# Performance work log

Hardware: AMD Instinct MI355X
Metric: run time of the kernel (lower is better)

The kernel has to match this reference:

```python
import jax, jax.numpy as jnp
import numpy as np

B, S, D = 2, 2048, 2048
H, HKV, HD = 32, 8, 64
G = H // HKV  # num_key_value_groups


def setup_inputs() -> dict:
    key = jax.random.key(0)
    ks = jax.random.split(key, 9)
    sc = 0.02
    return {
        "x": jax.random.normal(ks[0], (B, S, D), jnp.float32),
        "wq": jax.random.normal(ks[1], (H * HD, D), jnp.float32) * sc,
        "bq": jax.random.normal(ks[2], (H * HD,), jnp.float32) * sc,
        "wk": jax.random.normal(ks[3], (HKV * HD, D), jnp.float32) * sc,
        "bk": jax.random.normal(ks[4], (HKV * HD,), jnp.float32) * sc,
        "wv": jax.random.normal(ks[5], (HKV * HD, D), jnp.float32) * sc,
        "bv": jax.random.normal(ks[6], (HKV * HD,), jnp.float32) * sc,
        "wo": jax.random.normal(ks[7], (D, H * HD), jnp.float32) * sc,
        "bo": jax.random.normal(ks[8], (D,), jnp.float32) * sc,
    }


def reference(x, wq, bq, wk, bk, wv, bv, wo, bo):
    b, s, _ = x.shape
    # fused-QKV-style projections (nn.Linear: x @ W.T + b)
    q = (jnp.einsum("bsd,ed->bse", x, wq) + bq).reshape(b, s, H, HD)
    k = (jnp.einsum("bsd,ed->bse", x, wk) + bk).reshape(b, s, HKV, HD)
    v = (jnp.einsum("bsd,ed->bse", x, wv) + bv).reshape(b, s, HKV, HD)
    # (B, Hkv, G, S, hd): grouped query heads share a KV head — same math as
    # repeat_kv (expand+flatten) without materializing the expanded KV tensor
    q = q.transpose(0, 2, 1, 3).reshape(b, HKV, G, s, HD)
    k = k.transpose(0, 2, 1, 3)  # (B, Hkv, S, hd)
    v = v.transpose(0, 2, 1, 3)
    scale = 1.0 / jnp.sqrt(jnp.asarray(HD, x.dtype))
    scores = jnp.einsum("bkgqd,bktd->bkgqt", q, k) * scale  # (B,Hkv,G,S,S)
    causal = jnp.tril(jnp.ones((s, s), bool))
    scores = jnp.where(causal, scores, jnp.asarray(-jnp.inf, scores.dtype))
    probs = jax.nn.softmax(scores, axis=-1)
    o = jnp.einsum("bkgqt,bktd->bkgqd", probs, v)  # (B,Hkv,G,S,hd)
    o = o.reshape(b, H, s, HD).transpose(0, 2, 1, 3).reshape(b, s, H * HD)
    return jnp.einsum("bse,de->bsd", o, wo) + bo
```

## Files before the change

kernel.cpp:

```cpp
#include <hip/hip_runtime.h>
#include <hip/hip_bf16.h>
#include <cmath>

#define B_   2
#define S_   2048
#define D_   2048
#define H_   32
#define HKV_ 8
#define HD_  64

using bf16 = __hip_bfloat16;
typedef __bf16    bf16x8 __attribute__((ext_vector_type(8)));
typedef float     floatx4 __attribute__((ext_vector_type(4)));
typedef _Float16  half4 __attribute__((ext_vector_type(4)));
typedef _Float16  half8 __attribute__((ext_vector_type(8)));
typedef _Float16  half2v __attribute__((ext_vector_type(2)));

#if __has_builtin(__builtin_amdgcn_exp2f)
#define EXP2(x) __builtin_amdgcn_exp2f(x)
#else
#define EXP2(x) exp2f(x)
#endif

#define QSCALE 0.18033688011112042f

__device__ inline void async16(const void* g, void* l) {
  __builtin_amdgcn_global_load_lds(
      (const __attribute__((address_space(1))) void*)g,
      (__attribute__((address_space(3))) void*)l, 16, 0, 0);
}

__device__ inline half2v pkrtz(float a, float b) {
  return __builtin_bit_cast(half2v, __builtin_amdgcn_cvt_pkrtz(a, b));
}

#define MFMA32B(a, b, c) __builtin_amdgcn_mfma_f32_16x16x32_bf16((a), (b), (c), 0, 0, 0)
#define MFMA16H(a, b, c) __builtin_amdgcn_mfma_f32_16x16x16f16((a), (b), (c), 0, 0, 0)

#define BARX() { asm volatile("" ::: "memory"); __builtin_amdgcn_s_barrier(); \
                 asm volatile("" ::: "memory"); }
#define LGKM0() asm volatile("s_waitcnt lgkmcnt(0)" ::: "memory")

__global__ void f2b_all(const float* __restrict__ x,  const float* __restrict__ wq,
                        const float* __restrict__ wk, const float* __restrict__ wv,
                        const float* __restrict__ wo,
                        bf16* __restrict__ xb,  bf16* __restrict__ wqb,
                        bf16* __restrict__ wkb, bf16* __restrict__ wvb,
                        bf16* __restrict__ wob) {
  const int i = blockIdx.x * blockDim.x + threadIdx.x;
  const float* src; bf16* dst; int off; float scale = 1.0f;
  if (i < 1048576)      { src = x;  dst = xb;  off = 0; }
  else if (i < 1572864) { src = wq; dst = wqb; off = 1048576; scale = QSCALE; }
  else if (i < 1703936) { src = wk; dst = wkb; off = 1572864; }
  else if (i < 1835008) { src = wv; dst = wvb; off = 1703936; }
  else                  { src = wo; dst = wob; off = 1835008; }
  const int j = i - off;
  float4 a  = ((const float4*)src)[2 * j];
  float4 b2 = ((const float4*)src)[2 * j + 1];
  alignas(16) bf16 t[8];
  t[0] = __float2bfloat16(a.x * scale);  t[1] = __float2bfloat16(a.y * scale);
  t[2] = __float2bfloat16(a.z * scale);  t[3] = __float2bfloat16(a.w * scale);
  t[4] = __float2bfloat16(b2.x * scale); t[5] = __float2bfloat16(b2.y * scale);
  t[6] = __float2bfloat16(b2.z * scale); t[7] = __float2bfloat16(b2.w * scale);
  ((uint4*)dst)[j] = *(const uint4*)t;
}

__global__ __launch_bounds__(256, 2)
void gemm_qkv8(const bf16* __restrict__ xb, const bf16* __restrict__ Wcat,
               const float* __restrict__ bq, const float* __restrict__ bk,
               const float* __restrict__ bv,
               bf16* __restrict__ Qo, bf16* __restrict__ Ko,
               _Float16* __restrict__ VG) {
  constexpr int NT = D_ / 64;
  constexpr int BUFE = 20480;
  __shared__ bf16 L[2 * BUFE];

  const int id  = blockIdx.x;
  const int swz = (id & 7) * 64 + (id >> 3);
  const int bn  = swz >> 5;
  const int bm  = swz & 31;

  const int tid = threadIdx.x;
  const int wid = tid >> 6, lane = tid & 63;
  const int lm = lane & 15, quad = lane >> 4;
  const int wm = wid >> 1, wn = wid & 1;

  const int cOff = (quad * 8) ^ (((lm >> 3) & 1) << 4);
  const bf16* LA0 = L + (wm * 64 + lm) * 32 + cOff;
  const bf16* LB0 = L + 8192 + (wn * 96 + lm) * 32 + cOff;

  const int r0 = tid >> 2;
  const int csrc = ((tid & 3) * 8) ^ (((tid >> 5) & 1) << 4);
  const bf16* Asrc = xb   + (size_t)(bm * 128 + r0) * D_ + csrc;
  const bf16* Bsrc = Wcat + (size_t)(bn * 192 + r0) * D_ + csrc;
  bf16* Ld = L + tid * 8;

  floatx4 acc[4][6] = {};

#define STG_A(tt, hh, DB) { \
    async16(Asrc + (tt) * 64 + (hh) * 32,                  (DB) + (hh) * 4096); \
    async16(Asrc + (size_t)64 * D_ + (tt) * 64 + (hh) * 32, (DB) + (hh) * 4096 + 2048); }
#define STG_B(tt, hh, DB) { \
    async16(Bsrc + (tt) * 64 + (hh) * 32,                    (DB) + 8192 + (hh) * 6144); \
    async16(Bsrc + (size_t)64 * D_ + (tt) * 64 + (hh) * 32,  (DB) + 8192 + (hh) * 6144 + 2048); \
    async16(Bsrc + (size_t)128 * D_ + (tt) * 64 + (hh) * 32, (DB) + 8192 + (hh) * 6144 + 4096); }

  STG_A(0, 0, Ld); STG_B(0, 0, Ld);
  STG_A(0, 1, Ld); STG_B(0, 1, Ld);
  STG_A(1, 0, Ld + BUFE); STG_B(1, 0, Ld + BUFE);
  asm volatile("s_waitcnt vmcnt(10)" ::: "memory");
  BARX();

  auto tile = [&](int t, const int BUF) __attribute__((always_inline)) {
    const bf16* LA = LA0 + BUF;
    const bf16* LB = LB0 + BUF;
    bf16* SD  = Ld + BUF;
    bf16* SDo = Ld + (BUF ^ BUFE);
    const bool s1 = (t + 1) < NT, s2 = (t + 2) < NT;
    bf16x8 aF[4], bF[6];

#pragma unroll
    for (int i = 0; i < 4; ++i) aF[i] = *(const bf16x8*)(LA + i * 512);
#pragma unroll
    for (int i = 0; i < 6; ++i) bF[i] = *(const bf16x8*)(LB + i * 512);
    if (s1) { STG_A(t + 1, 1, SDo); STG_B(t + 1, 1, SDo); }
    BARX(); LGKM0();
    __builtin_amdgcn_s_setprio(1);
#pragma unroll
    for (int mi = 0; mi < 4; ++mi)
#pragma unroll
      for (int ni = 0; ni < 6; ++ni)
        acc[mi][ni] = MFMA32B(bF[ni], aF[mi], acc[mi][ni]);
    __builtin_amdgcn_s_setprio(0);
    if (s1) { asm volatile("s_waitcnt vmcnt(10)" ::: "memory"); }
    else    { asm volatile("s_waitcnt vmcnt(0)" ::: "memory"); }
    BARX();

#pragma unroll
    for (int i = 0; i < 4; ++i) aF[i] = *(const bf16x8*)(LA + 4096 + i * 512);
#pragma unroll
    for (int i = 0; i < 6; ++i) bF[i] = *(const bf16x8*)(LB + 6144 + i * 512);
    if (s2) { STG_A(t + 2, 0, SD); STG_B(t + 2, 0, SD); }
    BARX(); LGKM0();
    __builtin_amdgcn_s_setprio(1);
#pragma unroll
    for (int mi = 0; mi < 4; ++mi)
#pragma unroll
      for (int ni = 0; ni < 6; ++ni)
        acc[mi][ni] = MFMA32B(bF[ni], aF[mi], acc[mi][ni]);
    __builtin_amdgcn_s_setprio(0);
    if (s2)      { asm volatile("s_waitcnt vmcnt(10)" ::: "memory"); }
    else if (s1) { asm volatile("s_waitcnt vmcnt(5)" ::: "memory"); }
    else         { asm volatile("s_waitcnt vmcnt(0)" ::: "memory"); }
    BARX();
  };

  for (int t = 0; t < NT; t += 2) { tile(t, 0); tile(t + 1, BUFE); }

#undef STG_A
#undef STG_B

#pragma unroll
  for (int mi = 0; mi < 4; ++mi) {
    const int row = bm * 128 + wm * 64 + mi * 16 + lm;
#pragma unroll
    for (int ni = 0; ni < 6; ++ni) {
      const int colf = bn * 192 + wn * 96 + ni * 16;
      const int col0 = colf + quad * 4;
      if (colf < 2048) {
        float4 bv4 = *(const float4*)&bq[col0];
        alignas(8) bf16 t4[4];
#pragma unroll
        for (int r = 0; r < 4; ++r)
          t4[r] = __float2bfloat16(acc[mi][ni][r] + ((const float*)&bv4)[r] * QSCALE);
        *(uint2*)&Qo[(size_t)row * (H_ * HD_) + col0] = *(const uint2*)t4;
      } else if (colf < 2560) {
        const int ck = col0 - 2048;
        float4 bv4 = *(const float4*)&bk[ck];
        alignas(8) bf16 t4[4];
#pragma unroll
        for (int r = 0; r < 4; ++r)
          t4[r] = __float2bfloat16(acc[mi][ni][r] + ((const float*)&bv4)[r]);
        *(uint2*)&Ko[(size_t)row * (HKV_ * HD_) + ck] = *(const uint2*)t4;
      } else {
        const int cv = col0 - 2560;
        const int kvh = cv >> 6, hd = cv & 63;
        const int nh = hd >> 4;
        const int bb = row >> 11, s2 = row & 2047;
        const int tl = s2 >> 6, kvin = s2 & 63;
        const int kc = kvin >> 4, qd = (kvin >> 2) & 3, j = kvin & 3;
        const size_t base = ((size_t)((bb * 8 + kvh) * 32 + tl) << 12) +
                            (size_t)(((kc * 2 + (nh >> 1)) * 4 + qd) * 128 +
                                     (nh & 1) * 4 + j);
        float4 bv4 = *(const float4*)&bv[cv];
#pragma unroll
        for (int r = 0; r < 4; ++r)
          VG[base + (size_t)(quad * 4 + r) * 8] =
              (_Float16)(acc[mi][ni][r] + ((const float*)&bv4)[r]);
      }
    }
  }
}

__global__ __launch_bounds__(512, 2)
void gemm_o8(const bf16* __restrict__ A, const bf16* __restrict__ Bm,
             const float* __restrict__ bias, float* __restrict__ C) {
  constexpr int NT = D_ / 64;
  constexpr int BUFE = 24576;
  __shared__ bf16 L[2 * BUFE];

  const int id = blockIdx.x;
  const int bn = id & 7;
  const int bm = id >> 3;

  const int tid = threadIdx.x;
  const int wid = tid >> 6, lane = tid & 63;
  const int lm = lane & 15, quad = lane >> 4;
  const int wm = wid >> 2, wn = wid & 3;

  const int cOff = (quad * 8) ^ (((lm >> 3) & 1) << 4);
  const bf16* LA0 = L + (wm * 64 + lm) * 32 + cOff;
  const bf16* LB0 = L + 4096 + (wn * 64 + lm) * 32 + cOff;

  const int r0 = tid >> 2;
  const int csrc = ((tid & 3) * 8) ^ (((tid >> 5) & 1) << 4);
  const bf16* Asrc = A  + (size_t)(bm * 128 + r0) * D_ + csrc;
  const bf16* Bs0  = Bm + (size_t)(bn * 256 + r0) * D_ + csrc;
  const bf16* Bs1  = Bs0 + (size_t)128 * D_;
  bf16* Ld = L + tid * 8;

  floatx4 acc[4][4] = {};

#define STG_A(tt, hh, DB)  async16(Asrc + (tt) * 64 + (hh) * 32, (DB) + (hh) * 12288)
#define STG_B0(tt, hh, DB) async16(Bs0  + (tt) * 64 + (hh) * 32, (DB) + 4096 + (hh) * 12288)
#define STG_B1(tt, hh, DB) async16(Bs1  + (tt) * 64 + (hh) * 32, (DB) + 8192 + (hh) * 12288)

  STG_A(0, 0, Ld); STG_B0(0, 0, Ld); STG_B1(0, 0, Ld);
  STG_A(0, 1, Ld); STG_B0(0, 1, Ld); STG_B1(0, 1, Ld);
  STG_A(1, 0, Ld + BUFE); STG_B0(1, 0, Ld + BUFE); STG_B1(1, 0, Ld + BUFE);
  asm volatile("s_waitcnt vmcnt(6)" ::: "memory");
  BARX();

  auto tile = [&](int t, const int BUF) __attribute__((always_inline)) {
    const bf16* LA = LA0 + BUF;
    const bf16* LB = LB0 + BUF;
    bf16* SD  = Ld + BUF;
    bf16* SDo = Ld + (BUF ^ BUFE);
    const bool s1 = (t + 1) < NT, s2 = (t + 2) < NT;
    bf16x8 aF[4], bF[4];

#pragma unroll
    for (int i = 0; i < 4; ++i) aF[i] = *(const bf16x8*)(LA + i * 512);
#pragma unroll
    for (int i = 0; i < 4; ++i) bF[i] = *(const bf16x8*)(LB + i * 512);
    if (s1) { STG_A(t + 1, 1, SDo); STG_B0(t + 1, 1, SDo); STG_B1(t + 1, 1, SDo); }
    BARX(); LGKM0();
    __builtin_amdgcn_s_setprio(1);
#pragma unroll
    for (int mi = 0; mi < 4; ++mi)
#pragma unroll
      for (int ni = 0; ni < 4; ++ni)
        acc[mi][ni] = MFMA32B(bF[ni], aF[mi], acc[mi][ni]);
    __builtin_amdgcn_s_setprio(0);
    if (s1) { asm volatile("s_waitcnt vmcnt(6)" ::: "memory"); }
    else    { asm volatile("s_waitcnt vmcnt(0)" ::: "memory"); }
    BARX();

#pragma unroll
    for (int i = 0; i < 4; ++i) aF[i] = *(const bf16x8*)(LA + 12288 + i * 512);
#pragma unroll
    for (int i = 0; i < 4; ++i) bF[i] = *(const bf16x8*)(LB + 12288 + i * 512);
    if (s2) { STG_A(t + 2, 0, SD); STG_B0(t + 2, 0, SD); STG_B1(t + 2, 0, SD); }
    BARX(); LGKM0();
    __builtin_amdgcn_s_setprio(1);
#pragma unroll
    for (int mi = 0; mi < 4; ++mi)
#pragma unroll
      for (int ni = 0; ni < 4; ++ni)
        acc[mi][ni] = MFMA32B(bF[ni], aF[mi], acc[mi][ni]);
    __builtin_amdgcn_s_setprio(0);
    if (s2)      { asm volatile("s_waitcnt vmcnt(6)" ::: "memory"); }
    else if (s1) { asm volatile("s_waitcnt vmcnt(3)" ::: "memory"); }
    else         { asm volatile("s_waitcnt vmcnt(0)" ::: "memory"); }
    BARX();
  };

  for (int t = 0; t < NT; t += 2) { tile(t, 0); tile(t + 1, BUFE); }

#undef STG_A
#undef STG_B0
#undef STG_B1

#pragma unroll
  for (int mi = 0; mi < 4; ++mi) {
    const int row = bm * 128 + wm * 64 + mi * 16 + lm;
#pragma unroll
    for (int ni = 0; ni < 4; ++ni) {
      const int col0 = bn * 256 + wn * 64 + ni * 16 + quad * 4;
      float4 bv4 = *(const float4*)&bias[col0];
      float4 o4;
      o4.x = acc[mi][ni][0] + bv4.x; o4.y = acc[mi][ni][1] + bv4.y;
      o4.z = acc[mi][ni][2] + bv4.z; o4.w = acc[mi][ni][3] + bv4.w;
      *(float4*)&C[(size_t)row * D_ + col0] = o4;
    }
  }
}

__global__ __launch_bounds__(256, 5)
void attn_kernel(const bf16* __restrict__ Q, const bf16* __restrict__ K,
                 const _Float16* __restrict__ VG, bf16* __restrict__ O) {
  const int tid = threadIdx.x;
  const int wid = tid >> 6, lane = tid & 63;
  const int lm = lane & 15, quad = lane >> 4;

  const int n   = blockIdx.y * 64 + blockIdx.x;
  const int x3  = n & 7, b1 = (n >> 3) & 1;
  const int pair = n >> 4;
  const int grp  = x3 * 2 + b1;
  const int b    = grp >> 3, kvh = grp & 7;
  const int head = kvh * 4 + wid;

  const int hi = 127 - pair, lo = pair;
  const int nt_hi = (hi >> 2) + 1;
  const int nt_lo = (lo >> 2) + 1;

  __shared__ bf16     Ks[2 * 64 * 64];
  __shared__ _Float16 Vs[2 * 64 * 64];

  const int tb[2] = {hi * 16, lo * 16};

  bf16x8 qf[2][2];
#pragma unroll
  for (int tt = 0; tt < 2; ++tt) {
    const size_t qg = ((size_t)(b * S_ + tb[tt] + lm)) * (H_ * HD_) + head * HD_;
#pragma unroll
    for (int kf = 0; kf < 2; ++kf)
      qf[tt][kf] = *(const bf16x8*)&Q[qg + kf * 32 + quad * 8];
  }

  half4 onesh;
#pragma unroll
  for (int j = 0; j < 4; ++j) onesh[j] = (_Float16)1.0f;

  floatx4 o_acc[2][4] = {};
  floatx4 lacc[2] = {};

  auto stage = [&](int t, int buf) {
    const int tr = tid >> 2;
    const int tc = (tid & 3) * 8;
#pragma unroll
    for (int c = 0; c < 2; ++c) {
      async16(&K[(size_t)(b * S_ + t * 64 + tr) * (HKV_ * HD_) + kvh * HD_ + c * 32 + tc],
              &Ks[buf * 4096 + c * 2048 + tid * 8]);
      async16(&VG[((size_t)(grp * 32 + t) << 12) + c * 2048 + tid * 8],
              &Vs[buf * 4096 + c * 2048 + tid * 8]);
    }
  };

  stage(0, 0);

  for (int t = 0; t < nt_hi; ++t) {
    const int cur = t & 1;
    asm volatile("s_waitcnt vmcnt(0)" ::: "memory");
    __syncthreads();
    if (t + 1 < nt_hi) stage(t + 1, cur ^ 1);

    const bf16*     Kb = &Ks[cur * 4096];
    const _Float16* Vb = &Vs[cur * 4096];
    const int t0 = t * 64;
    const int nact = (t < nt_lo) ? 2 : 1;

    int kcmax[2], kcross[2];
#pragma unroll
    for (int tt = 0; tt < 2; ++tt) {
      const int rel = tb[tt] + 15 - t0;
      kcmax[tt]  = (tt < nact) ? ((rel >> 4) >= 3 ? 4 : (rel >> 4) + 1) : 0;
      kcross[tt] = rel >> 4;
    }

    half4 ps[2] = {};

#pragma unroll
    for (int kc = 0; kc < 4; ++kc) {
      if (kc >= kcmax[0]) break;
      bf16x8 kb0 = *(const bf16x8*)&Kb[(kc * 16 + lm) * 32 + quad * 8];
      bf16x8 kb1 = *(const bf16x8*)&Kb[2048 + (kc * 16 + lm) * 32 + quad * 8];

      floatx4 sT[2];
      __builtin_amdgcn_s_setprio(1);
#pragma unroll
      for (int tt = 0; tt < 2; ++tt) {
        if (kc >= kcmax[tt]) continue;
        floatx4 s0 = {};
        s0 = MFMA32B(kb0, qf[tt][0], s0);
        sT[tt] = MFMA32B(kb1, qf[tt][1], s0);
      }
      __builtin_amdgcn_s_setprio(0);

      half8 v0 = *(const half8*)&Vb[(kc * 8 + quad) * 128 + lm * 8];
      half8 v1 = *(const half8*)&Vb[(kc * 8 + 4 + quad) * 128 + lm * 8];
      half4 v0l = __builtin_shufflevector(v0, v0, 0, 1, 2, 3);
      half4 v0h = __builtin_shufflevector(v0, v0, 4, 5, 6, 7);
      half4 v1l = __builtin_shufflevector(v1, v1, 0, 1, 2, 3);
      half4 v1h = __builtin_shufflevector(v1, v1, 4, 5, 6, 7);

      half4 pbk[2];
#pragma unroll
      for (int tt = 0; tt < 2; ++tt) {
        if (kc >= kcmax[tt]) continue;
        floatx4 s = sT[tt];
        if (kc == kcross[tt]) {
          const int qrel = tb[tt] + lm - t0;
#pragma unroll
          for (int r = 0; r < 4; ++r)
            if (kc * 16 + quad * 4 + r > qrel) s[r] = -__builtin_inff();
        }
        half2v c0 = pkrtz(EXP2(s[0]), EXP2(s[1]));
        half2v c1 = pkrtz(EXP2(s[2]), EXP2(s[3]));
        half4 pk = __builtin_shufflevector(c0, c1, 0, 1, 2, 3);
        pbk[tt] = pk;
        ps[tt] += pk;
      }

      __builtin_amdgcn_s_setprio(1);
#pragma unroll
      for (int tt = 0; tt < 2; ++tt) {
        if (kc >= kcmax[tt]) continue;
        o_acc[tt][0] = MFMA16H(v0l, pbk[tt], o_acc[tt][0]);
        o_acc[tt][1] = MFMA16H(v0h, pbk[tt], o_acc[tt][1]);
        o_acc[tt][2] = MFMA16H(v1l, pbk[tt], o_acc[tt][2]);
        o_acc[tt][3] = MFMA16H(v1h, pbk[tt], o_acc[tt][3]);
      }
      __builtin_amdgcn_s_setprio(0);
    }

#pragma unroll
    for (int tt = 0; tt < 2; ++tt)
      if (kcmax[tt]) lacc[tt] = MFMA16H(onesh, ps[tt], lacc[tt]);
  }

#pragma unroll
  for (int tt = 0; tt < 2; ++tt) {
    const float rl = 1.f / lacc[tt][0];
    const size_t rowg = (size_t)(b * S_ + tb[tt] + lm);
#pragma unroll
    for (int nh = 0; nh < 4; ++nh) {
      alignas(8) bf16 tmp[4];
#pragma unroll
      for (int r = 0; r < 4; ++r)
        tmp[r] = __float2bfloat16(o_acc[tt][nh][r] * rl);
      *(uint2*)&O[rowg * (H_ * HD_) + head * HD_ + nh * 16 + quad * 4] = *(uint2*)tmp;
    }
  }
}

extern "C" void kernel_launch(void* const* d_in, const int* in_sizes, int n_in,
                              void* d_out, int out_size, void* d_ws, size_t ws_size,
                              hipStream_t stream) {
  (void)in_sizes; (void)n_in; (void)out_size; (void)ws_size;
  const float* x  = (const float*)d_in[0];
  const float* wq = (const float*)d_in[1];
  const float* bq = (const float*)d_in[2];
  const float* wk = (const float*)d_in[3];
  const float* bk = (const float*)d_in[4];
  const float* wv = (const float*)d_in[5];
  const float* bv = (const float*)d_in[6];
  const float* wo = (const float*)d_in[7];
  const float* bo = (const float*)d_in[8];
  float* out = (float*)d_out;

  const int M = B_ * S_;
  const int E = H_ * HD_;
  const int EKV = HKV_ * HD_;

  char* ws = (char*)d_ws;
  size_t off = 0;
  auto alloc = [&](size_t bytes) {
    char* p = ws + off;
    off += (bytes + 255) & ~(size_t)255;
    return p;
  };
  bf16* xb   = (bf16*)alloc((size_t)M * D_ * 2);
  bf16* Wcat = (bf16*)alloc((size_t)(E + 2 * EKV) * D_ * 2);
  bf16* wob  = (bf16*)alloc((size_t)D_ * E * 2);
  bf16* Qb   = (bf16*)alloc((size_t)M * E * 2);
  bf16* Kb   = (bf16*)alloc((size_t)M * EKV * 2);
  _Float16* VG = (_Float16*)alloc((size_t)M * EKV * 2);
  bf16* Ob   = (bf16*)alloc((size_t)M * E * 2);

  bf16* wqb = Wcat;
  bf16* wkb = Wcat + (size_t)E * D_;
  bf16* wvb = Wcat + (size_t)(E + EKV) * D_;

  f2b_all<<<9216, 256, 0, stream>>>(x, wq, wk, wv, wo, xb, wqb, wkb, wvb, wob);

  gemm_qkv8<<<dim3(512), dim3(256), 0, stream>>>(xb, Wcat, bq, bk, bv,
                                                 Qb, Kb, VG);

  attn_kernel<<<dim3(64, 16), 256, 0, stream>>>(Qb, Kb, VG, Ob);

  gemm_o8<<<dim3(256), dim3(512), 0, stream>>>(Ob, wob, bo, out);
}
```

Measured before the change: 288.8 us.

## Rewrite QKV GEMM with per-wave private LDS buffers and no block barriers

The QKV projection GEMM now gives each of the four waves its own shared-memory region. Each wave stages its own 64-row slice of x plus the full 192-column weight tile, so the main loop needs no block-wide barriers, only per-wave waitcnt. Tiles grow to 256x192 per block with a 32-wide K step and double buffering, and occupancy drops to one block per CU. Because every wave loads the same weight tile separately, global and LDS traffic for the weights rises in exchange for removing synchronization, and the grid halves to 256 blocks.

After: 291.6 us. Within noise of the previous version (+1.0%).

```diff
diff --git a/kernel.cpp b/kernel.cpp
--- a/kernel.cpp
+++ b/kernel.cpp
@@ -65,107 +65,79 @@
   ((uint4*)dst)[j] = *(const uint4*)t;
 }
 
-__global__ __launch_bounds__(256, 2)
-void gemm_qkv8(const bf16* __restrict__ xb, const bf16* __restrict__ Wcat,
-               const float* __restrict__ bq, const float* __restrict__ bk,
-               const float* __restrict__ bv,
-               bf16* __restrict__ Qo, bf16* __restrict__ Ko,
-               _Float16* __restrict__ VG) {
-  constexpr int NT = D_ / 64;
-  constexpr int BUFE = 20480;
-  __shared__ bf16 L[2 * BUFE];
-
-  const int id  = blockIdx.x;
-  const int swz = (id & 7) * 64 + (id >> 3);
-  const int bn  = swz >> 5;
-  const int bm  = swz & 31;
+__global__ __launch_bounds__(256, 1)
+void gemm_qkvbf(const bf16* __restrict__ xb, const bf16* __restrict__ Wcat,
+                const float* __restrict__ bq, const float* __restrict__ bk,
+                const float* __restrict__ bv,
+                bf16* __restrict__ Qo, bf16* __restrict__ Ko,
+                _Float16* __restrict__ VG) {
+  constexpr int NT = D_ / 32;
+  constexpr int WBUF = 16384;
+  __shared__ bf16 L[4 * WBUF];
+
+  const int id = blockIdx.x;
+  const int bm = id >> 4;
+  const int bn = id & 15;
 
   const int tid = threadIdx.x;
   const int wid = tid >> 6, lane = tid & 63;
   const int lm = lane & 15, quad = lane >> 4;
-  const int wm = wid >> 1, wn = wid & 1;
+
+  const int rl   = lane >> 2;
+  const int csrc = ((lane & 3) * 8) ^ (((lane >> 5) & 1) << 4);
+  const bf16* Asrc = xb   + (size_t)(bm * 256 + wid * 64 + rl) * D_ + csrc;
+  const bf16* Bsrc = Wcat + (size_t)(bn * 192 + rl) * D_ + csrc;
+  bf16* Ld = L + wid * WBUF + lane * 8;
 
   const int cOff = (quad * 8) ^ (((lm >> 3) & 1) << 4);
-  const bf16* LA0 = L + (wm * 64 + lm) * 32 + cOff;
-  const bf16* LB0 = L + 8192 + (wn * 96 + lm) * 32 + cOff;
-
-  const int r0 = tid >> 2;
-  const int csrc = ((tid & 3) * 8) ^ (((tid >> 5) & 1) << 4);
-  const bf16* Asrc = xb   + (size_t)(bm * 128 + r0) * D_ + csrc;
-  const bf16* Bsrc = Wcat + (size_t)(bn * 192 + r0) * D_ + csrc;
-  bf16* Ld = L + tid * 8;
-
-  floatx4 acc[4][6] = {};
-
-#define STG_A(tt, hh, DB) { \
-    async16(Asrc + (tt) * 64 + (hh) * 32,                  (DB) + (hh) * 4096); \
-    async16(Asrc + (size_t)64 * D_ + (tt) * 64 + (hh) * 32, (DB) + (hh) * 4096 + 2048); }
-#define STG_B(tt, hh, DB) { \
-    async16(Bsrc + (tt) * 64 + (hh) * 32,                    (DB) + 8192 + (hh) * 6144); \
-    async16(Bsrc + (size_t)64 * D_ + (tt) * 64 + (hh) * 32,  (DB) + 8192 + (hh) * 6144 + 2048); \
-    async16(Bsrc + (size_t)128 * D_ + (tt) * 64 + (hh) * 32, (DB) + 8192 + (hh) * 6144 + 4096); }
-
-  STG_A(0, 0, Ld); STG_B(0, 0, Ld);
-  STG_A(0, 1, Ld); STG_B(0, 1, Ld);
-  STG_A(1, 0, Ld + BUFE); STG_B(1, 0, Ld + BUFE);
-  asm volatile("s_waitcnt vmcnt(10)" ::: "memory");
-  BARX();
-
-  auto tile = [&](int t, const int BUF) __attribute__((always_inline)) {
-    const bf16* LA = LA0 + BUF;
-    const bf16* LB = LB0 + BUF;
-    bf16* SD  = Ld + BUF;
-    bf16* SDo = Ld + (BUF ^ BUFE);
-    const bool s1 = (t + 1) < NT, s2 = (t + 2) < NT;
-    bf16x8 aF[4], bF[6];
-
-#pragma unroll
-    for (int i = 0; i < 4; ++i) aF[i] = *(const bf16x8*)(LA + i * 512);
-#pragma unroll
-    for (int i = 0; i < 6; ++i) bF[i] = *(const bf16x8*)(LB + i * 512);
-    if (s1) { STG_A(t + 1, 1, SDo); STG_B(t + 1, 1, SDo); }
-    BARX(); LGKM0();
+  const bf16* LW = L + wid * WBUF + lm * 32 + cOff;
+
+  floatx4 acc[4][12] = {};
+
+#define STG(t) { \
+    const size_t ko = (size_t)(t) * 32; \
+    bf16* db = Ld + ((t) & 1) * 8192; \
+    async16(Asrc + ko,                    db); \
+    async16(Asrc + ko + (size_t)16 * D_,  db + 512); \
+    async16(Asrc + ko + (size_t)32 * D_,  db + 1024); \
+    async16(Asrc + ko + (size_t)48 * D_,  db + 1536); \
+    _Pragma("unroll") \
+    for (int j = 0; j < 12; ++j) \
+      async16(Bsrc + ko + (size_t)(j * 16) * D_, db + 2048 + j * 512); }
+
+  STG(0); STG(1);
+
+  for (int t = 0; t < NT; ++t) {
+    if (t + 1 < NT) { asm volatile("s_waitcnt vmcnt(16)" ::: "memory"); }
+    else            { asm volatile("s_waitcnt vmcnt(0)"  ::: "memory"); }
+
+    const bf16* LA = LW + (t & 1) * 8192;
+    const bf16* LB = LA + 2048;
+    bf16x8 aF[4], bF[12];
+#pragma unroll
+    for (int i = 0; i < 4; ++i)  aF[i] = *(const bf16x8*)(LA + i * 512);
+#pragma unroll
+    for (int i = 0; i < 12; ++i) bF[i] = *(const bf16x8*)(LB + i * 512);
+    LGKM0();
+
+    if (t + 2 < NT) STG(t + 2);
+
     __builtin_amdgcn_s_setprio(1);
 #pragma unroll
     for (int mi = 0; mi < 4; ++mi)
 #pragma unroll
-      for (int ni = 0; ni < 6; ++ni)
+      for (int ni = 0; ni < 12; ++ni)
         acc[mi][ni] = MFMA32B(bF[ni], aF[mi], acc[mi][ni]);
     __builtin_amdgcn_s_setprio(0);
-    if (s1) { asm volatile("s_waitcnt vmcnt(10)" ::: "memory"); }
-    else    { asm volatile("s_waitcnt vmcnt(0)" ::: "memory"); }
-    BARX();
-
-#pragma unroll
-    for (int i = 0; i < 4; ++i) aF[i] = *(const bf16x8*)(LA + 4096 + i * 512);
-#pragma unroll
-    for (int i = 0; i < 6; ++i) bF[i] = *(const bf16x8*)(LB + 6144 + i * 512);
-    if (s2) { STG_A(t + 2, 0, SD); STG_B(t + 2, 0, SD); }
-    BARX(); LGKM0();
-    __builtin_amdgcn_s_setprio(1);
-#pragma unroll
-    for (int mi = 0; mi < 4; ++mi)
-#pragma unroll
-      for (int ni = 0; ni < 6; ++ni)
-        acc[mi][ni] = MFMA32B(bF[ni], aF[mi], acc[mi][ni]);
-    __builtin_amdgcn_s_setprio(0);
-    if (s2)      { asm volatile("s_waitcnt vmcnt(10)" ::: "memory"); }
-    else if (s1) { asm volatile("s_waitcnt vmcnt(5)" ::: "memory"); }
-    else         { asm volatile("s_waitcnt vmcnt(0)" ::: "memory"); }
-    BARX();
-  };
-
-  for (int t = 0; t < NT; t += 2) { tile(t, 0); tile(t + 1, BUFE); }
-
-#undef STG_A
-#undef STG_B
+  }
+#undef STG
 
 #pragma unroll
   for (int mi = 0; mi < 4; ++mi) {
-    const int row = bm * 128 + wm * 64 + mi * 16 + lm;
-#pragma unroll
-    for (int ni = 0; ni < 6; ++ni) {
-      const int colf = bn * 192 + wn * 96 + ni * 16;
+    const int row = bm * 256 + wid * 64 + mi * 16 + lm;
+#pragma unroll
+    for (int ni = 0; ni < 12; ++ni) {
+      const int colf = bn * 192 + ni * 16;
       const int col0 = colf + quad * 4;
       if (colf < 2048) {
         float4 bv4 = *(const float4*)&bq[col0];
@@ -494,8 +466,8 @@
 
   f2b_all<<<9216, 256, 0, stream>>>(x, wq, wk, wv, wo, xb, wqb, wkb, wvb, wob);
 
-  gemm_qkv8<<<dim3(512), dim3(256), 0, stream>>>(xb, Wcat, bq, bk, bv,
-                                                 Qb, Kb, VG);
+  gemm_qkvbf<<<dim3(256), dim3(256), 0, stream>>>(xb, Wcat, bq, bk, bv,
+                                                  Qb, Kb, VG);
 
   attn_kernel<<<dim3(64, 16), 256, 0, stream>>>(Qb, Kb, VG, Ob);
 
```
